# Kernel tuning notes

Hardware: AMD Instinct MI355X
Metric: run time of the kernel (lower is better)

## Reference

```python
import jax, jax.numpy as jnp
import numpy as np

N, DIM, QK, HEADS, NWIN, TOPK = 1, 128, 128, 8, 8, 4
D = H = W = 32


def setup_inputs() -> dict:
    key = jax.random.key(0)
    ks = jax.random.split(key, 3)
    s = lambda fan: 1.0 / np.sqrt(fan)
    return {
        "x": jax.random.normal(ks[0], (N, D, H, W, DIM), jnp.float32),
        "w_qkv": jax.random.normal(ks[1], (DIM, 2 * QK + DIM), jnp.float32) * s(DIM),
        "b_qkv": jnp.zeros((2 * QK + DIM,), jnp.float32),
        "w_o": jax.random.normal(ks[2], (DIM, DIM), jnp.float32) * s(DIM),
        "b_o": jnp.zeros((DIM,), jnp.float32),
    }


def _forward(x, w_qkv, b_qkv, w_o, b_o):
    n, Dd, Hh, Ww, C = x.shape
    d, h, w = Dd // NWIN, Hh // NWIN, Ww // NWIN
    p3, w3 = NWIN ** 3, d * h * w
    cq, cv = QK // HEADS, DIM // HEADS
    scale = QK ** -0.5
    # window partition: n (q d)(j h)(i w) c -> n (q j i) d h w c
    xw = x.reshape(n, NWIN, d, NWIN, h, NWIN, w, C)
    xw = xw.transpose(0, 1, 3, 5, 2, 4, 6, 7).reshape(n, p3, d, h, w, C)
    # fused qkv projection
    qkv = xw @ w_qkv + b_qkv
    q, k, v = qkv[..., :QK], qkv[..., QK:2 * QK], qkv[..., 2 * QK:]
    q_pix = q.reshape(n, p3, w3, QK)
    kv_pix = jnp.concatenate([k, v], axis=-1).reshape(n, p3, w3, QK + DIM)
    # region-level routing (non-differentiable: detached in original)
    q_win = jax.lax.stop_gradient(q.mean((2, 3, 4)))  # (n, p3, QK)
    k_win = jax.lax.stop_gradient(k.mean((2, 3, 4)))
    logits = jnp.einsum('npc,nqc->npq', q_win * scale, k_win)  # (n, p3, p3)
    _, r_idx = jax.lax.top_k(logits, TOPK)  # (n, p3, topk)
    # gather top-k regions' KV per query window: (n, p3, topk, w3, QK+DIM)
    kv_sel = jax.vmap(lambda kvp, idx: kvp[idx])(kv_pix, r_idx)
    k_sel = kv_sel[..., :QK].reshape(n * p3, TOPK * w3, HEADS, cq).transpose(0, 2, 3, 1)  # (np3, m, cq, k*w3)
    v_sel = kv_sel[..., QK:].reshape(n * p3, TOPK * w3, HEADS, cv).transpose(0, 2, 1, 3)  # (np3, m, k*w3, cv)
    qh = q_pix.reshape(n * p3, w3, HEADS, cq).transpose(0, 2, 1, 3)  # (np3, m, w3, cq)
    attn = jax.nn.softmax((qh * scale) @ k_sel, axis=-1)  # (np3, m, w3, k*w3)
    out = attn @ v_sel  # (np3, m, w3, cv)
    # (n q j i) m (d h w) c -> n (q d)(j h)(i w)(m c)
    out = out.reshape(n, NWIN, NWIN, NWIN, HEADS, d, h, w, cv)
    out = out.transpose(0, 1, 5, 2, 6, 3, 7, 4, 8).reshape(n, Dd, Hh, Ww, DIM)
    out = out @ w_o + b_o
    return out, q, k, v


def reference(x, w_qkv, b_qkv, w_o, b_o):
    return _forward(x, w_qkv, b_qkv, w_o, b_o)
```

## Files before the change

kernel.cpp:

```cpp
#include <hip/hip_runtime.h>
#include <cmath>

namespace {

typedef __attribute__((ext_vector_type(8))) short short8;
typedef __attribute__((ext_vector_type(4))) float f32x4;
typedef __attribute__((ext_vector_type(4))) unsigned u32x4;

constexpr float kScale = 0.08838834764831845f;

__device__ __forceinline__ int voxel_row(int p, int pix) {
  int pd = p >> 6, ph = (p >> 3) & 7, pw = p & 7;
  int iz = pix >> 4, iy = (pix >> 2) & 3, ix = pix & 3;
  return (((pd * 4 + iz) * 32 + (ph * 4 + iy)) * 32 + (pw * 4 + ix));
}

__device__ __forceinline__ float dot4(float4 a, float4 b) {
  return a.x * b.x + a.y * b.y + a.z * b.z + a.w * b.w;
}

__device__ __forceinline__ short bf16c(float f) {
  unsigned u = __builtin_bit_cast(unsigned, f);
  u += 0x7fffu + ((u >> 16) & 1u);
  return (short)(u >> 16);
}

__device__ __forceinline__ unsigned bfpack(float lo, float hi) {
  return (unsigned)(unsigned short)bf16c(lo) |
         ((unsigned)(unsigned short)bf16c(hi) << 16);
}

__global__ __launch_bounds__(64) void k_pack2(
    const float* __restrict__ wqkv, const float* __restrict__ wo,
    short* __restrict__ dstq, short* __restrict__ dsto) {
  const int lane = threadIdx.x;
  const float* w;
  short* dst;
  int fid, N;
  if (blockIdx.x < 96) {
    w = wqkv; dst = dstq; fid = blockIdx.x; N = 384;
  } else {
    w = wo; dst = dsto; fid = blockIdx.x - 96; N = 128;
  }
  const int ntile = fid >> 2, ks = fid & 3;
  const int k0 = ks * 32 + (lane >> 4) * 8, col = ntile * 16 + (lane & 15);
  short8 o;
#pragma unroll
  for (int i = 0; i < 8; ++i) o[i] = bf16c(w[(size_t)(k0 + i) * N + col]);
  *(short8*)(dst + ((size_t)fid * 64 + lane) * 8) = o;
}

__global__ __launch_bounds__(512, 4) void k_qkv(
    const float* __restrict__ x, const short* __restrict__ wpk,
    const float* __restrict__ bias, const float* __restrict__ wfull,
    float* __restrict__ q, float* __restrict__ k, float* __restrict__ v,
    short* __restrict__ vt, short* __restrict__ kbh, short* __restrict__ qbh,
    float* __restrict__ qwin, float* __restrict__ kwin) {
  __shared__ short sX[64][136];
  __shared__ float xpart[8][16][8];
  __shared__ float xm[128];
  const int p = blockIdx.x, t = threadIdx.x;
  const int wave = t >> 6, lane = t & 63, l15 = lane & 15, lg = lane >> 4;

  float ps[8] = {0.f, 0.f, 0.f, 0.f, 0.f, 0.f, 0.f, 0.f};
#pragma unroll
  for (int r = 0; r < 2; ++r) {
    int unit = t + r * 512;
    int row = unit >> 4, u = unit & 15;
    const float* src = x + (size_t)voxel_row(p, row) * 128 + u * 8;
    float4 a = *(const float4*)src, b = *(const float4*)(src + 4);
    ps[0] += a.x; ps[1] += a.y; ps[2] += a.z; ps[3] += a.w;
    ps[4] += b.x; ps[5] += b.y; ps[6] += b.z; ps[7] += b.w;
    short8 o;
    o[0] = bf16c(a.x); o[1] = bf16c(a.y); o[2] = bf16c(a.z); o[3] = bf16c(a.w);
    o[4] = bf16c(b.x); o[5] = bf16c(b.y); o[6] = bf16c(b.z); o[7] = bf16c(b.w);
    *(short8*)(&sX[row][u * 8]) = o;
  }
#pragma unroll
  for (int i = 0; i < 8; ++i) {
    ps[i] += __shfl_xor(ps[i], 16);
    ps[i] += __shfl_xor(ps[i], 32);
  }
  if (lg == 0)
#pragma unroll
    for (int i = 0; i < 8; ++i) xpart[wave][l15][i] = ps[i];
  __syncthreads();
  if (t < 128) {
    float s = 0.f;
#pragma unroll
    for (int w8 = 0; w8 < 8; ++w8) s += xpart[w8][t >> 3][t & 7];
    xm[t] = s * (1.f / 64.f);
  }

  f32x4 acc[4][3];
#pragma unroll
  for (int mt = 0; mt < 4; ++mt)
#pragma unroll
    for (int nt = 0; nt < 3; ++nt) acc[mt][nt] = f32x4{0.f, 0.f, 0.f, 0.f};
#pragma unroll
  for (int ks = 0; ks < 4; ++ks) {
    short8 a[4];
#pragma unroll
    for (int mt = 0; mt < 4; ++mt)
      a[mt] = *(const short8*)(&sX[mt * 16 + l15][ks * 32 + lg * 8]);
#pragma unroll
    for (int nt = 0; nt < 3; ++nt) {
      int ntg = wave * 3 + nt;
      short8 b = *(const short8*)(wpk + ((size_t)(ntg * 4 + ks) * 64 + lane) * 8);
#pragma unroll
      for (int mt = 0; mt < 4; ++mt)
        acc[mt][nt] = __builtin_amdgcn_mfma_f32_16x16x32_bf16(a[mt], b, acc[mt][nt], 0, 0, 0);
    }
  }
#pragma unroll
  for (int nt = 0; nt < 3; ++nt) {
    int n = (wave * 3 + nt) * 16 + l15;
    float bv = bias[n];
    float* dst = n < 128 ? q : (n < 256 ? k : v);
    int col = n & 127;
#pragma unroll
    for (int mt = 0; mt < 4; ++mt) {
      float o0 = acc[mt][nt][0] + bv, o1 = acc[mt][nt][1] + bv;
      float o2 = acc[mt][nt][2] + bv, o3 = acc[mt][nt][3] + bv;
      int row0 = mt * 16 + lg * 4;
      dst[(size_t)(p * 64 + row0 + 0) * 128 + col] = o0;
      dst[(size_t)(p * 64 + row0 + 1) * 128 + col] = o1;
      dst[(size_t)(p * 64 + row0 + 2) * 128 + col] = o2;
      dst[(size_t)(p * 64 + row0 + 3) * 128 + col] = o3;
      if (n >= 256) {
        uint2 pk;
        pk.x = bfpack(o0, o1);
        pk.y = bfpack(o2, o3);
        *(uint2*)(vt + (size_t)p * 8192 + (size_t)(n - 256) * 64 + row0) = pk;
      } else if (n >= 128) {
        int hh = (n - 128) >> 4, d = (n - 128) & 15;
        short* kd = kbh + (((size_t)(p * 8 + hh)) * 64 + row0) * 16 + d;
        kd[0] = bf16c(o0);
        kd[16] = bf16c(o1);
        kd[32] = bf16c(o2);
        kd[48] = bf16c(o3);
      } else {
        int hh = n >> 4, d = n & 15;
        short* qd = qbh + (((size_t)(p * 8 + hh)) * 64 + row0) * 16 + d;
        qd[0] = bf16c(o0 * kScale);
        qd[16] = bf16c(o1 * kScale);
        qd[32] = bf16c(o2 * kScale);
        qd[48] = bf16c(o3 * kScale);
      }
    }
  }

  __syncthreads();
  if (t < 256) {
    float acc2 = bias[t];
    for (int kk = 0; kk < 128; ++kk)
      acc2 = fmaf(xm[kk], wfull[(size_t)kk * 384 + t], acc2);
    if (t < 128) qwin[p * 128 + t] = acc2;
    else kwin[p * 128 + (t - 128)] = acc2;
  }
}

__global__ __launch_bounds__(512, 4) void k_attn(
    const short* __restrict__ qbh, const short* __restrict__ kbh,
    const short* __restrict__ vt, const float* __restrict__ qwin,
    const float* __restrict__ kwin, const short* __restrict__ wpk_o,
    const float* __restrict__ b_o, float* __restrict__ out) {
  __shared__ float lgits[512];
  __shared__ float rv[256];
  __shared__ int ri[256];
  __shared__ float qs[128];
  __shared__ int widx[4];
  __shared__ short sO[64][136];

  const int p = blockIdx.x, t = threadIdx.x;
  const int h = t >> 6, lane = t & 63;
  const int l15 = lane & 15, lg = lane >> 4;

  const short* qw = qbh + ((size_t)(p * 8 + h)) * 1024;
  short8 qf[4];
#pragma unroll
  for (int nt = 0; nt < 4; ++nt) {
    if (lg < 2)
      qf[nt] = *(const short8*)(qw + (nt * 16 + l15) * 16 + lg * 8);
    else
      qf[nt] = short8{0, 0, 0, 0, 0, 0, 0, 0};
  }

  if (t < 32) *(float4*)(&qs[t * 4]) = *(const float4*)(qwin + p * 128 + t * 4);
  __syncthreads();
  {
    const float* kr = kwin + (size_t)t * 128;
    float s = 0.f;
    for (int c = 0; c < 128; c += 4)
      s += dot4(*(const float4*)(qs + c), *(const float4*)(kr + c));
    lgits[t] = s;
  }
  __syncthreads();
  for (int sel = 0; sel < 4; ++sel) {
    if (t < 256) {
      float bv = lgits[t];
      int bi = t;
      float v2 = lgits[t + 256];
      if (v2 > bv) { bv = v2; bi = t + 256; }
      rv[t] = bv; ri[t] = bi;
    }
    __syncthreads();
    for (int off = 128; off > 0; off >>= 1) {
      if (t < off && rv[t + off] > rv[t]) { rv[t] = rv[t + off]; ri[t] = ri[t + off]; }
      __syncthreads();
    }
    if (t == 0) { widx[sel] = ri[0]; lgits[ri[0]] = -INFINITY; }
    __syncthreads();
  }

  const int src0 = ((lg & 1) << 5) | l15;
  const int src1 = src0 + 16;

  float m_r[4] = {-1e30f, -1e30f, -1e30f, -1e30f};
  float l_r[4] = {0.f, 0.f, 0.f, 0.f};
  f32x4 oacc[4];
#pragma unroll
  for (int i = 0; i < 4; ++i) oacc[i] = f32x4{0.f, 0.f, 0.f, 0.f};

#pragma unroll
  for (int c = 0; c < 4; ++c) {
    const int wsel = widx[c];
    const short* kw = kbh + ((size_t)(wsel * 8 + h)) * 1024;
    short8 af[4];
#pragma unroll
    for (int mt = 0; mt < 4; ++mt) {
      if (lg < 2)
        af[mt] = *(const short8*)(kw + (mt * 16 + l15) * 16 + lg * 8);
      else
        af[mt] = short8{0, 0, 0, 0, 0, 0, 0, 0};
    }
    const short* vw = vt + (size_t)wsel * 8192 + (size_t)(h * 16 + l15) * 64 + lg * 8;
    short8 av0 = *(const short8*)(vw);
    short8 av1 = *(const short8*)(vw + 32);

#pragma unroll
    for (int nt = 0; nt < 4; ++nt) {
      f32x4 s[4];
#pragma unroll
      for (int mt = 0; mt < 4; ++mt)
        s[mt] = __builtin_amdgcn_mfma_f32_16x16x32_bf16(
            af[mt], qf[nt], f32x4{0.f, 0.f, 0.f, 0.f}, 0, 0, 0);
      float mx = -1e30f;
#pragma unroll
      for (int mt = 0; mt < 4; ++mt)
#pragma unroll
        for (int j = 0; j < 4; ++j) mx = fmaxf(mx, s[mt][j]);
      mx = fmaxf(mx, __shfl_xor(mx, 16));
      mx = fmaxf(mx, __shfl_xor(mx, 32));
      float mnew = fmaxf(m_r[nt], mx);
      float sc = __expf(m_r[nt] - mnew);
      m_r[nt] = mnew;
      float ls = 0.f;
#pragma unroll
      for (int mt = 0; mt < 4; ++mt)
#pragma unroll
        for (int j = 0; j < 4; ++j) {
          float e = __expf(s[mt][j] - mnew);
          s[mt][j] = e;
          ls += e;
        }
      ls += __shfl_xor(ls, 16);
      ls += __shfl_xor(ls, 32);
      l_r[nt] = l_r[nt] * sc + ls;
      oacc[nt][0] *= sc; oacc[nt][1] *= sc;
      oacc[nt][2] *= sc; oacc[nt][3] *= sc;
      unsigned P2[4][2];
#pragma unroll
      for (int mt = 0; mt < 4; ++mt) {
        P2[mt][0] = bfpack(s[mt][0], s[mt][1]);
        P2[mt][1] = bfpack(s[mt][2], s[mt][3]);
      }
#pragma unroll
      for (int kt = 0; kt < 2; ++kt) {
        unsigned lo0 = (unsigned)__shfl((int)P2[2 * kt + 0][0], src0);
        unsigned hi0 = (unsigned)__shfl((int)P2[2 * kt + 1][0], src0);
        unsigned lo1 = (unsigned)__shfl((int)P2[2 * kt + 0][1], src0);
        unsigned hi1 = (unsigned)__shfl((int)P2[2 * kt + 1][1], src0);
        unsigned lo2 = (unsigned)__shfl((int)P2[2 * kt + 0][0], src1);
        unsigned hi2 = (unsigned)__shfl((int)P2[2 * kt + 1][0], src1);
        unsigned lo3 = (unsigned)__shfl((int)P2[2 * kt + 0][1], src1);
        unsigned hi3 = (unsigned)__shfl((int)P2[2 * kt + 1][1], src1);
        u32x4 bw;
        bw[0] = (lg < 2) ? lo0 : hi0;
        bw[1] = (lg < 2) ? lo1 : hi1;
        bw[2] = (lg < 2) ? lo2 : hi2;
        bw[3] = (lg < 2) ? lo3 : hi3;
        short8 bfr = __builtin_bit_cast(short8, bw);
        oacc[nt] = __builtin_amdgcn_mfma_f32_16x16x32_bf16(
            kt == 0 ? av0 : av1, bfr, oacc[nt], 0, 0, 0);
      }
    }
  }

#pragma unroll
  for (int nt = 0; nt < 4; ++nt) {
    float inv = 1.f / l_r[nt];
    uint2 pk;
    pk.x = bfpack(oacc[nt][0] * inv, oacc[nt][1] * inv);
    pk.y = bfpack(oacc[nt][2] * inv, oacc[nt][3] * inv);
    *(uint2*)(&sO[nt * 16 + l15][h * 16 + lg * 4]) = pk;
  }
  __syncthreads();

  f32x4 pacc[4];
#pragma unroll
  for (int mt = 0; mt < 4; ++mt) pacc[mt] = f32x4{0.f, 0.f, 0.f, 0.f};
#pragma unroll
  for (int ks = 0; ks < 4; ++ks) {
    short8 a[4];
#pragma unroll
    for (int mt = 0; mt < 4; ++mt)
      a[mt] = *(const short8*)(&sO[mt * 16 + l15][ks * 32 + lg * 8]);
    short8 b = *(const short8*)(wpk_o + ((size_t)(h * 4 + ks) * 64 + lane) * 8);
#pragma unroll
    for (int mt = 0; mt < 4; ++mt)
      pacc[mt] = __builtin_amdgcn_mfma_f32_16x16x32_bf16(a[mt], b, pacc[mt], 0, 0, 0);
  }
  {
    int n = h * 16 + l15;
    float bv = b_o[n];
#pragma unroll
    for (int mt = 0; mt < 4; ++mt)
#pragma unroll
      for (int j = 0; j < 4; ++j)
        out[(size_t)voxel_row(p, mt * 16 + lg * 4 + j) * 128 + n] = pacc[mt][j] + bv;
  }
}

}

extern "C" void kernel_launch(void* const* d_in, const int* in_sizes, int n_in,
                              void* d_out, int out_size, void* d_ws, size_t ws_size,
                              hipStream_t stream) {
  (void)in_sizes; (void)n_in; (void)out_size; (void)ws_size;
  const float* x = (const float*)d_in[0];
  const float* w_qkv = (const float*)d_in[1];
  const float* b_qkv = (const float*)d_in[2];
  const float* w_o = (const float*)d_in[3];
  const float* b_o = (const float*)d_in[4];

  float* out = (float*)d_out;
  float* q = out + 4194304;
  float* k = q + 4194304;
  float* v = k + 4194304;

  float* qwin = (float*)d_ws;
  float* kwin = qwin + 65536;
  short* wpk_qkv = (short*)(kwin + 65536);
  short* wpk_o = wpk_qkv + 49152;
  short* vt = wpk_o + 16384;
  short* kbh = vt + 4194304;
  short* qbh = kbh + 4194304;

  k_pack2<<<128, 64, 0, stream>>>(w_qkv, w_o, wpk_qkv, wpk_o);
  k_qkv<<<512, 512, 0, stream>>>(x, wpk_qkv, b_qkv, w_qkv, q, k, v, vt, kbh, qbh, qwin, kwin);
  k_attn<<<512, 512, 0, stream>>>(qbh, kbh, vt, qwin, kwin, wpk_o, b_o, out);
}
```

Baseline: 78.45 us.

## Use wave-level shuffle top-k, exp2 softmax, and paired score MFMAs

Replaces the shared-memory tree reduction for top-k window selection, which needed many block-wide barriers, with a single-wavefront register/shuffle argmax over the 512 logits. Folds log2(e) into the stored Q scale so the softmax can use exp2f instead of __expf. Issues score MFMAs for two query tiles together so more independent matrix ops can be in flight before the softmax math. The tie-break now prefers the lower index, which could differ from the old selection only on exact ties.

```diff
diff --git a/kernel.cpp b/kernel.cpp
--- a/kernel.cpp
+++ b/kernel.cpp
@@ -8,6 +8,7 @@
 typedef __attribute__((ext_vector_type(4))) unsigned u32x4;
 
 constexpr float kScale = 0.08838834764831845f;
+constexpr float kScaleL2 = 0.12751744900764504f;
 
 __device__ __forceinline__ int voxel_row(int p, int pix) {
   int pd = p >> 6, ph = (p >> 3) & 7, pw = p & 7;
@@ -142,10 +143,10 @@
       } else {
         int hh = n >> 4, d = n & 15;
         short* qd = qbh + (((size_t)(p * 8 + hh)) * 64 + row0) * 16 + d;
-        qd[0] = bf16c(o0 * kScale);
-        qd[16] = bf16c(o1 * kScale);
-        qd[32] = bf16c(o2 * kScale);
-        qd[48] = bf16c(o3 * kScale);
+        qd[0] = bf16c(o0 * kScaleL2);
+        qd[16] = bf16c(o1 * kScaleL2);
+        qd[32] = bf16c(o2 * kScaleL2);
+        qd[48] = bf16c(o3 * kScaleL2);
       }
     }
   }
@@ -166,8 +167,6 @@
     const float* __restrict__ kwin, const short* __restrict__ wpk_o,
     const float* __restrict__ b_o, float* __restrict__ out) {
   __shared__ float lgits[512];
-  __shared__ float rv[256];
-  __shared__ int ri[256];
   __shared__ float qs[128];
   __shared__ int widx[4];
   __shared__ short sO[64][136];
@@ -196,22 +195,29 @@
     lgits[t] = s;
   }
   __syncthreads();
-  for (int sel = 0; sel < 4; ++sel) {
-    if (t < 256) {
-      float bv = lgits[t];
-      int bi = t;
-      float v2 = lgits[t + 256];
-      if (v2 > bv) { bv = v2; bi = t + 256; }
-      rv[t] = bv; ri[t] = bi;
-    }
-    __syncthreads();
-    for (int off = 128; off > 0; off >>= 1) {
-      if (t < off && rv[t + off] > rv[t]) { rv[t] = rv[t + off]; ri[t] = ri[t + off]; }
-      __syncthreads();
-    }
-    if (t == 0) { widx[sel] = ri[0]; lgits[ri[0]] = -INFINITY; }
-    __syncthreads();
-  }
+  if (h == 0) {
+    float vals[8];
+#pragma unroll
+    for (int i = 0; i < 8; ++i) vals[i] = lgits[lane * 8 + i];
+    for (int sel = 0; sel < 4; ++sel) {
+      float bv = -1e30f;
+      int bi = 0;
+#pragma unroll
+      for (int i = 0; i < 8; ++i) {
+        int idx = lane * 8 + i;
+        if (vals[i] > bv) { bv = vals[i]; bi = idx; }
+      }
+#pragma unroll
+      for (int off = 32; off > 0; off >>= 1) {
+        float ov = __shfl_xor(bv, off);
+        int oi = __shfl_xor(bi, off);
+        if (ov > bv || (ov == bv && oi < bi)) { bv = ov; bi = oi; }
+      }
+      if (lane == 0) widx[sel] = bi;
+      if ((bi >> 3) == lane) vals[bi & 7] = -1e30f;
+    }
+  }
+  __syncthreads();
 
   const int src0 = ((lg & 1) << 5) | l15;
   const int src1 = src0 + 16;
@@ -239,60 +245,69 @@
     short8 av1 = *(const short8*)(vw + 32);
 
 #pragma unroll
-    for (int nt = 0; nt < 4; ++nt) {
-      f32x4 s[4];
+    for (int np = 0; np < 2; ++np) {
+      f32x4 s[4][2];
 #pragma unroll
       for (int mt = 0; mt < 4; ++mt)
-        s[mt] = __builtin_amdgcn_mfma_f32_16x16x32_bf16(
-            af[mt], qf[nt], f32x4{0.f, 0.f, 0.f, 0.f}, 0, 0, 0);
-      float mx = -1e30f;
-#pragma unroll
-      for (int mt = 0; mt < 4; ++mt)
-#pragma unroll
-        for (int j = 0; j < 4; ++j) mx = fmaxf(mx, s[mt][j]);
-      mx = fmaxf(mx, __shfl_xor(mx, 16));
-      mx = fmaxf(mx, __shfl_xor(mx, 32));
-      float mnew = fmaxf(m_r[nt], mx);
-      float sc = __expf(m_r[nt] - mnew);
-      m_r[nt] = mnew;
-      float ls = 0.f;
-#pragma unroll
-      for (int mt = 0; mt < 4; ++mt)
-#pragma unroll
-        for (int j = 0; j < 4; ++j) {
-          float e = __expf(s[mt][j] - mnew);
-          s[mt][j] = e;
-          ls += e;
+#pragma unroll
+        for (int j2 = 0; j2 < 2; ++j2)
+          s[mt][j2] = __builtin_amdgcn_mfma_f32_16x16x32_bf16(
+              af[mt], qf[np * 2 + j2], f32x4{0.f, 0.f, 0.f, 0.f}, 0, 0, 0);
+
+#pragma unroll
+      for (int j2 = 0; j2 < 2; ++j2) {
+        const int nt = np * 2 + j2;
+        float mx = -1e30f;
+#pragma unroll
+        for (int mt = 0; mt < 4; ++mt)
+#pragma unroll
+          for (int j = 0; j < 4; ++j) mx = fmaxf(mx, s[mt][j2][j]);
+        mx = fmaxf(mx, __shfl_xor(mx, 16));
+        mx = fmaxf(mx, __shfl_xor(mx, 32));
+        float mnew = fmaxf(m_r[nt], mx);
+        float sc = exp2f(m_r[nt] - mnew);
+        m_r[nt] = mnew;
+        l_r[nt] *= sc;
+        oacc[nt][0] *= sc; oacc[nt][1] *= sc;
+        oacc[nt][2] *= sc; oacc[nt][3] *= sc;
+        float ls = 0.f;
+#pragma unroll
+        for (int mt = 0; mt < 4; ++mt)
+#pragma unroll
+          for (int j = 0; j < 4; ++j) {
+            float e = exp2f(s[mt][j2][j] - m_r[nt]);
+            s[mt][j2][j] = e;
+            ls += e;
+          }
+        ls += __shfl_xor(ls, 16);
+        ls += __shfl_xor(ls, 32);
+        l_r[nt] += ls;
+
+        unsigned P2[4][2];
+#pragma unroll
+        for (int mt = 0; mt < 4; ++mt) {
+          P2[mt][0] = bfpack(s[mt][j2][0], s[mt][j2][1]);
+          P2[mt][1] = bfpack(s[mt][j2][2], s[mt][j2][3]);
         }
-      ls += __shfl_xor(ls, 16);
-      ls += __shfl_xor(ls, 32);
-      l_r[nt] = l_r[nt] * sc + ls;
-      oacc[nt][0] *= sc; oacc[nt][1] *= sc;
-      oacc[nt][2] *= sc; oacc[nt][3] *= sc;
-      unsigned P2[4][2];
-#pragma unroll
-      for (int mt = 0; mt < 4; ++mt) {
-        P2[mt][0] = bfpack(s[mt][0], s[mt][1]);
-        P2[mt][1] = bfpack(s[mt][2], s[mt][3]);
-      }
-#pragma unroll
-      for (int kt = 0; kt < 2; ++kt) {
-        unsigned lo0 = (unsigned)__shfl((int)P2[2 * kt + 0][0], src0);
-        unsigned hi0 = (unsigned)__shfl((int)P2[2 * kt + 1][0], src0);
-        unsigned lo1 = (unsigned)__shfl((int)P2[2 * kt + 0][1], src0);
-        unsigned hi1 = (unsigned)__shfl((int)P2[2 * kt + 1][1], src0);
-        unsigned lo2 = (unsigned)__shfl((int)P2[2 * kt + 0][0], src1);
-        unsigned hi2 = (unsigned)__shfl((int)P2[2 * kt + 1][0], src1);
-        unsigned lo3 = (unsigned)__shfl((int)P2[2 * kt + 0][1], src1);
-        unsigned hi3 = (unsigned)__shfl((int)P2[2 * kt + 1][1], src1);
-        u32x4 bw;
-        bw[0] = (lg < 2) ? lo0 : hi0;
-        bw[1] = (lg < 2) ? lo1 : hi1;
-        bw[2] = (lg < 2) ? lo2 : hi2;
-        bw[3] = (lg < 2) ? lo3 : hi3;
-        short8 bfr = __builtin_bit_cast(short8, bw);
-        oacc[nt] = __builtin_amdgcn_mfma_f32_16x16x32_bf16(
-            kt == 0 ? av0 : av1, bfr, oacc[nt], 0, 0, 0);
+#pragma unroll
+        for (int kt = 0; kt < 2; ++kt) {
+          unsigned lo0 = (unsigned)__shfl((int)P2[2 * kt + 0][0], src0);
+          unsigned hi0 = (unsigned)__shfl((int)P2[2 * kt + 1][0], src0);
+          unsigned lo1 = (unsigned)__shfl((int)P2[2 * kt + 0][1], src0);
+          unsigned hi1 = (unsigned)__shfl((int)P2[2 * kt + 1][1], src0);
+          unsigned lo2 = (unsigned)__shfl((int)P2[2 * kt + 0][0], src1);
+          unsigned hi2 = (unsigned)__shfl((int)P2[2 * kt + 1][0], src1);
+          unsigned lo3 = (unsigned)__shfl((int)P2[2 * kt + 0][1], src1);
+          unsigned hi3 = (unsigned)__shfl((int)P2[2 * kt + 1][1], src1);
+          u32x4 bw;
+          bw[0] = (lg < 2) ? lo0 : hi0;
+          bw[1] = (lg < 2) ? lo1 : hi1;
+          bw[2] = (lg < 2) ? lo2 : hi2;
+          bw[3] = (lg < 2) ? lo3 : hi3;
+          short8 bfr = __builtin_bit_cast(short8, bw);
+          oacc[nt] = __builtin_amdgcn_mfma_f32_16x16x32_bf16(
+              kt == 0 ? av0 : av1, bfr, oacc[nt], 0, 0, 0);
+        }
       }
     }
   }
```

New measurement: 83.64 us. 1.07x slower.
